# Performance work log

Measured on AMD Instinct MI355X. Metric: run time of the kernel, lower is better.

The kernel has to match this reference:

```python
import jax, jax.numpy as jnp
import numpy as np

B, S, E = 4, 1024, 1024
H, DH = 16, 64
P = 64  # prompt length
MASKED_BIAS = -10000.0


def setup_inputs() -> dict:
    key = jax.random.key(0)
    ks = jax.random.split(key, 9)
    return {
        "hidden_states": jax.random.normal(ks[0], (B, S, E), jnp.float32),
        "promptKey": jax.random.normal(ks[1], (B, H, P, DH), jnp.float32),
        "promptValue": jax.random.normal(ks[2], (B, H, P, DH), jnp.float32),
        "textualKey": jax.random.normal(ks[3], (B, H, S, DH), jnp.float32),
        "textualValue": jax.random.normal(ks[4], (B, H, S, DH), jnp.float32),
        "promptMask": jnp.ones((B, 1, S, P), jnp.bool_),
        "c_attn_w": jax.random.normal(ks[5], (E, 3 * E), jnp.float32) * 0.02,
        "c_attn_b": jnp.zeros((3 * E,), jnp.float32),
        "c_proj_w": jax.random.normal(ks[6], (E, E), jnp.float32) * 0.02,
        "c_proj_b": jnp.zeros((E,), jnp.float32),
    }


def _split_heads(t):
    # [B, S, E] -> [B, H, S, DH]
    b, s, _ = t.shape
    return t.reshape(b, s, H, DH).transpose(0, 2, 1, 3)


def reference(hidden_states, promptKey, promptValue, textualKey, textualValue,
              promptMask, c_attn_w, c_attn_b, c_proj_w, c_proj_b):
    qkv = hidden_states @ c_attn_w + c_attn_b          # [B,S,3E]
    q, k, v = jnp.split(qkv, 3, axis=-1)
    q, k, v = _split_heads(q), _split_heads(k), _split_heads(v)  # [B,H,S,DH]

    # scores against prompt KV, textual KV, and elementwise self term
    promptW = jnp.einsum("bhsd,bhpd->bhsp", q, promptKey)       # [B,H,S,P]
    textW = jnp.einsum("bhsd,bhtd->bhst", q, textualKey)        # [B,H,S,S]
    selfW = jnp.sum(q * k, axis=-1, keepdims=True)              # [B,H,S,1]
    attn_weights = jnp.concatenate((promptW, textW, selfW), axis=-1)
    attn_weights = attn_weights / jnp.sqrt(jnp.float32(DH))

    # non-residual causal mask: bias[qlen-qlen:qlen, 1:klen+1] -> strictly lower tri
    causal = jnp.tri(S, S, -1, dtype=bool)                      # [S,S]
    self_mask = jnp.ones((S, 1), dtype=bool)
    causal_self = jnp.concatenate((causal, self_mask), axis=-1)[None, None]  # [1,1,S,S+1]
    full_mask = jnp.concatenate(
        (promptMask, jnp.broadcast_to(causal_self, (B, 1, S, S + 1))), axis=-1)
    attn_weights = jnp.where(full_mask, attn_weights, MASKED_BIAS)
    attn_weights = jax.nn.softmax(attn_weights, axis=-1)

    wSelf = attn_weights[..., -1:]                              # [B,H,S,1]
    wRest = attn_weights[..., :-1]                              # [B,H,S,P+S]
    valuePast = jnp.concatenate((promptValue, textualValue), axis=-2)  # [B,H,P+S,DH]
    attn_output = jnp.einsum("bhsk,bhkd->bhsd", wRest, valuePast) + wSelf * v

    # merge heads and output projection
    attn_output = attn_output.transpose(0, 2, 1, 3).reshape(B, S, E)
    return attn_output @ c_proj_w + c_proj_b
```

## Files before the change

### kernel.cpp

```cpp
#include <hip/hip_runtime.h>
#include <hip/hip_bf16.h>
#include <stdint.h>

#define H_ 16
#define DH_ 64
#define S_ 1024
#define B_ 4
#define E_ 1024
#define P_ 64
#define BH_ (B_ * H_)
#define KV_ (P_ + S_)
#define NT_ 17
#define TILE_ELEMS 4096

typedef __attribute__((ext_vector_type(8))) short short8;
typedef __attribute__((ext_vector_type(4))) float floatx4;

#define MFMA_BF16(a, b, c) __builtin_amdgcn_mfma_f32_16x16x32_bf16((a), (b), (c), 0, 0, 0)

__device__ __forceinline__ float bf2f(unsigned short u) {
    union { float f; uint32_t i; } x;
    x.i = ((uint32_t)u) << 16;
    return x.f;
}
__device__ __forceinline__ unsigned short f2bf(float f) {
    uint32_t i = __float_as_uint(f);
    uint32_t r = (i + 0x7fffu + ((i >> 16) & 1u)) >> 16;
    return (unsigned short)r;
}

__device__ __forceinline__ void gl_lds16(const void* g, void* l) {
    __builtin_amdgcn_global_load_lds(
        (const __attribute__((address_space(1))) uint32_t*)g,
        (__attribute__((address_space(3))) uint32_t*)l, 16, 0, 0);
}

#define BARRIER() asm volatile("s_barrier" ::: "memory")
#define WAIT_VM(n) asm volatile("s_waitcnt vmcnt(" #n ")" ::: "memory")
#define LGKM0() asm volatile("s_waitcnt lgkmcnt(0)" ::: "memory")

__global__ void prep(const float* __restrict__ hidden, const float* __restrict__ cw,
                     const float* __restrict__ pw, const float* __restrict__ pK,
                     const float* __restrict__ tK, const float* __restrict__ pV,
                     const float* __restrict__ tV, unsigned short* __restrict__ Ah,
                     unsigned short* __restrict__ Wt1, unsigned short* __restrict__ Wt2,
                     unsigned short* __restrict__ Kp, unsigned short* __restrict__ Vp) {
    __shared__ float t[32][33];
    int bid = blockIdx.x, tid = threadIdx.x;
    if (bid < 4096) {
        int i = bid * 256 + tid;
        float4 v = ((const float4*)hidden)[i];
        ushort4 o;
        o.x = f2bf(v.x); o.y = f2bf(v.y); o.z = f2bf(v.z); o.w = f2bf(v.w);
        ((ushort4*)Ah)[i] = o;
    } else if (bid < 8192) {
        const float* in; unsigned short* out; int R, C, bxx, byy;
        if (bid < 7168) { int i = bid - 4096; in = cw; out = Wt1; R = 1024; C = 3072; bxx = i % 96; byy = i / 96; }
        else            { int i = bid - 7168; in = pw; out = Wt2; R = 1024; C = 1024; bxx = i % 32; byy = i / 32; }
        int tx = tid & 31, ty = tid >> 5;
        int c0 = bxx * 32, r0 = byy * 32;
#pragma unroll
        for (int i = 0; i < 4; ++i)
            t[ty + i * 8][tx] = in[(size_t)(r0 + ty + i * 8) * C + c0 + tx];
        __syncthreads();
#pragma unroll
        for (int i = 0; i < 4; ++i)
            out[(size_t)(c0 + ty + i * 8) * R + r0 + tx] = f2bf(t[tx][ty + i * 8]);
    } else {
        int gid0 = (bid - 8192) * 256 + tid;
        int half = gid0 / (BH_ * 8704);
        int gid = gid0 % (BH_ * 8704);
        int bh = gid / 8704, rem = gid % 8704;
        int tt = rem / 512, r2 = rem % 512;
        int f = r2 >> 6, lane = r2 & 63;
        int nt = f >> 1, h = f & 1, quad = lane >> 4, cl = lane & 15;
        unsigned short o[8];
        if (half == 0) {
            int key = tt * 64 + nt * 16 + cl;
            int dh = h * 32 + quad * 8;
            const float* src = (key < P_)
                ? pK + ((size_t)bh * P_ + key) * DH_ + dh
                : tK + ((size_t)bh * S_ + (key - P_)) * DH_ + dh;
#pragma unroll
            for (int u = 0; u < 8; ++u) o[u] = f2bf(src[u]);
            *(int4*)&Kp[(size_t)gid * 8] = *(int4*)o;
        } else {
            int dhn = nt * 16 + cl;
            int kbase = tt * 64 + h * 32 + quad * 8;
            const float* src = (kbase < P_)
                ? pV + ((size_t)bh * P_ + kbase) * DH_ + dhn
                : tV + ((size_t)bh * S_ + (kbase - P_)) * DH_ + dhn;
#pragma unroll
            for (int u = 0; u < 8; ++u) o[u] = f2bf(src[(size_t)u * DH_]);
            *(int4*)&Vp[(size_t)gid * 8] = *(int4*)o;
        }
    }
}

template <int MODE, int TM, int TN, int BK>
__global__ __launch_bounds__(256) void gemm_bt(
    const unsigned short* __restrict__ A, const unsigned short* __restrict__ Bt,
    const float* __restrict__ bias, float* __restrict__ Cout,
    unsigned short* __restrict__ Qo, unsigned short* __restrict__ Ko,
    unsigned short* __restrict__ Vo, int M, int N, int K) {
    constexpr int MI = TM / 32, NI = TN / 32;
    constexpr int NA = TM * BK / 2048;
    constexpr int NB = TN * BK / 2048;
    static_assert(NA + NB == 4, "vmcnt constant assumes 4 loads/tile");
    __shared__ __align__(16) unsigned short lA[2][TM * BK];
    __shared__ __align__(16) unsigned short lB[2][TN * BK];
    int tid = threadIdx.x;
    int wave = tid >> 6, lane = tid & 63, quad = lane >> 4, cl = lane & 15;
    int m0 = blockIdx.y * TM, n0 = blockIdx.x * TN;
    int wm = (wave >> 1) * (TM / 2), wn = (wave & 1) * (TN / 2);
    floatx4 acc[MI][NI];
#pragma unroll
    for (int mi = 0; mi < MI; ++mi)
#pragma unroll
        for (int ni = 0; ni < NI; ++ni) acc[mi][ni] = (floatx4){0.f, 0.f, 0.f, 0.f};

    auto issue = [&](int k0, int buf) {
#pragma unroll
        for (int li = 0; li < NA; ++li) {
            int o = (li * 256 + tid) * 16;
            int hh = o / (TM * 64), rr = (o % (TM * 64)) >> 6, c8 = (o >> 4) & 3;
            gl_lds16(A + (size_t)(m0 + rr) * K + k0 + hh * 32 + c8 * 8,
                     (char*)lA[buf] + o);
        }
#pragma unroll
        for (int li = 0; li < NB; ++li) {
            int o = (li * 256 + tid) * 16;
            int hh = o / (TN * 64), rr = (o % (TN * 64)) >> 6, c8 = (o >> 4) & 3;
            gl_lds16(Bt + (size_t)(n0 + rr) * K + k0 + hh * 32 + c8 * 8,
                     (char*)lB[buf] + o);
        }
    };
    auto compute = [&](int buf) {
#pragma unroll
        for (int kk = 0; kk < BK / 32; ++kk) {
            short8 af[MI], bfr[NI];
#pragma unroll
            for (int mi = 0; mi < MI; ++mi)
                af[mi] = *(const short8*)&lA[buf][kk * TM * 32 + (wm + mi * 16 + cl) * 32 + quad * 8];
#pragma unroll
            for (int ni = 0; ni < NI; ++ni)
                bfr[ni] = *(const short8*)&lB[buf][kk * TN * 32 + (wn + ni * 16 + cl) * 32 + quad * 8];
#pragma unroll
            for (int mi = 0; mi < MI; ++mi)
#pragma unroll
                for (int ni = 0; ni < NI; ++ni)
                    acc[mi][ni] = MFMA_BF16(af[mi], bfr[ni], acc[mi][ni]);
        }
    };

    int nT = K / BK;
    issue(0, 0);
    for (int t = 0; t < nT; ++t) {
        int buf = t & 1;
        if (t + 1 < nT) {
            issue((t + 1) * BK, buf ^ 1);
            WAIT_VM(4);
        } else {
            WAIT_VM(0);
        }
        BARRIER();
        compute(buf);
        BARRIER();
    }

#pragma unroll
    for (int ni = 0; ni < NI; ++ni) {
        int ncol = n0 + wn + ni * 16 + cl;
        float bv = bias[ncol];
#pragma unroll
        for (int mi = 0; mi < MI; ++mi) {
#pragma unroll
            for (int r = 0; r < 4; ++r) {
                int mrow = m0 + wm + mi * 16 + quad * 4 + r;
                float v = acc[mi][ni][r] + bv;
                if (MODE == 0) {
                    Cout[(size_t)mrow * N + ncol] = v;
                } else {
                    int which = ncol >> 10, e = ncol & 1023;
                    int hh = e >> 6, dh = e & 63;
                    int b = mrow >> 10, s = mrow & 1023;
                    size_t idx = ((size_t)(b * H_ + hh) * S_ + s) * DH_ + dh;
                    unsigned short* dst = (which == 0) ? Qo : ((which == 1) ? Ko : Vo);
                    dst[idx] = f2bf(v);
                }
            }
        }
    }
}

__global__ __launch_bounds__(512, 2) void gemm8_qkv(
    const unsigned short* __restrict__ A, const unsigned short* __restrict__ Bt,
    const float* __restrict__ bias, unsigned short* __restrict__ Qo,
    unsigned short* __restrict__ Ko, unsigned short* __restrict__ Vo,
    int M, int N, int K, int nbx) {
    __shared__ __align__(16) unsigned short sm[4][16384];
    int tid = threadIdx.x;
    int wave = tid >> 6, lane = tid & 63, quad = lane >> 4, cl = lane & 15;
    int cpx = gridDim.x >> 3;
    int swzb = ((int)blockIdx.x & 7) * cpx + ((int)blockIdx.x >> 3);
    int m0 = (swzb / nbx) * 256, n0 = (swzb % nbx) * 256;
    int wm = (wave >> 2) * 128, wn = (wave & 3) * 64;
    int cq = quad ^ ((cl >> 1) & 3);

    auto stage = [&](const unsigned short* __restrict__ G, int row0, int k0,
                     unsigned short* l) {
#pragma unroll
        for (int li = 0; li < 4; ++li) {
            int idx = li * 512 + tid;
            int kh = idx >> 10;
            int r = (idx >> 2) & 255;
            int c = (idx & 3) ^ ((r >> 1) & 3);
            gl_lds16(G + (size_t)(row0 + r) * K + k0 + kh * 32 + c * 8,
                     (char*)l + idx * 16);
        }
    };

    floatx4 acc[8][4];
#pragma unroll
    for (int mi = 0; mi < 8; ++mi)
#pragma unroll
        for (int ni = 0; ni < 4; ++ni) acc[mi][ni] = (floatx4){0.f, 0.f, 0.f, 0.f};

    int nT = K / 64;
    stage(A, m0, 0, sm[0]);
    stage(Bt, n0, 0, sm[1]);
    WAIT_VM(0);
    BARRIER();

    for (int j = 0; j < nT; ++j) {
        const unsigned short* sa = sm[(j & 1) * 2];
        const unsigned short* sb = sm[(j & 1) * 2 + 1];
        unsigned short* na = sm[((j & 1) ^ 1) * 2];
        unsigned short* nb = sm[((j & 1) ^ 1) * 2 + 1];
        short8 af[4], bf0[4], bf1[4];

#pragma unroll
        for (int ni = 0; ni < 4; ++ni)
            bf0[ni] = *(const short8*)(sb + (wn + ni * 16 + cl) * 32 + cq * 8);
#pragma unroll
        for (int mi = 0; mi < 4; ++mi)
            af[mi] = *(const short8*)(sa + (wm + mi * 16 + cl) * 32 + cq * 8);
        if (j + 1 < nT) stage(A, m0, (j + 1) * 64, na);
        BARRIER(); LGKM0();
        __builtin_amdgcn_s_setprio(1);
#pragma unroll
        for (int mi = 0; mi < 4; ++mi)
#pragma unroll
            for (int ni = 0; ni < 4; ++ni)
                acc[mi][ni] = MFMA_BF16(af[mi], bf0[ni], acc[mi][ni]);
        __builtin_amdgcn_s_setprio(0);
        BARRIER();

#pragma unroll
        for (int ni = 0; ni < 4; ++ni)
            bf1[ni] = *(const short8*)(sb + 8192 + (wn + ni * 16 + cl) * 32 + cq * 8);
#pragma unroll
        for (int mi = 0; mi < 4; ++mi)
            af[mi] = *(const short8*)(sa + 8192 + (wm + mi * 16 + cl) * 32 + cq * 8);
        if (j + 1 < nT) stage(Bt, n0, (j + 1) * 64, nb);
        BARRIER(); LGKM0();
        __builtin_amdgcn_s_setprio(1);
#pragma unroll
        for (int mi = 0; mi < 4; ++mi)
#pragma unroll
            for (int ni = 0; ni < 4; ++ni)
                acc[mi][ni] = MFMA_BF16(af[mi], bf1[ni], acc[mi][ni]);
        __builtin_amdgcn_s_setprio(0);
        BARRIER();

#pragma unroll
        for (int mi = 0; mi < 4; ++mi)
            af[mi] = *(const short8*)(sa + (wm + 64 + mi * 16 + cl) * 32 + cq * 8);
        BARRIER(); LGKM0();
        __builtin_amdgcn_s_setprio(1);
#pragma unroll
        for (int mi = 0; mi < 4; ++mi)
#pragma unroll
            for (int ni = 0; ni < 4; ++ni)
                acc[4 + mi][ni] = MFMA_BF16(af[mi], bf0[ni], acc[4 + mi][ni]);
        __builtin_amdgcn_s_setprio(0);
        BARRIER();

#pragma unroll
        for (int mi = 0; mi < 4; ++mi)
            af[mi] = *(const short8*)(sa + 8192 + (wm + 64 + mi * 16 + cl) * 32 + cq * 8);
        BARRIER(); LGKM0();
        __builtin_amdgcn_s_setprio(1);
#pragma unroll
        for (int mi = 0; mi < 4; ++mi)
#pragma unroll
            for (int ni = 0; ni < 4; ++ni)
                acc[4 + mi][ni] = MFMA_BF16(af[mi], bf1[ni], acc[4 + mi][ni]);
        __builtin_amdgcn_s_setprio(0);
        WAIT_VM(0);
        BARRIER();
    }

#pragma unroll
    for (int ni = 0; ni < 4; ++ni) {
        int ncol = n0 + wn + ni * 16 + cl;
        float bv = bias[ncol];
        int which = ncol >> 10, e = ncol & 1023;
        int hh = e >> 6, dh = e & 63;
        unsigned short* dst = (which == 0) ? Qo : ((which == 1) ? Ko : Vo);
#pragma unroll
        for (int mi = 0; mi < 8; ++mi) {
#pragma unroll
            for (int r = 0; r < 4; ++r) {
                int mrow = m0 + wm + mi * 16 + quad * 4 + r;
                int b = mrow >> 10, s = mrow & 1023;
                dst[((size_t)(b * H_ + hh) * S_ + s) * DH_ + dh] =
                    f2bf(acc[mi][ni][r] + bv);
            }
        }
    }
}

__global__ __launch_bounds__(256) void attn_k(
    const unsigned short* __restrict__ Q, const unsigned short* __restrict__ Kc,
    const unsigned short* __restrict__ Vc, const unsigned short* __restrict__ Kp,
    const unsigned short* __restrict__ Vp, unsigned short* __restrict__ Aout) {
    __shared__ __align__(16) unsigned short lK[2][TILE_ELEMS];
    __shared__ __align__(16) unsigned short lV[2][TILE_ELEMS];
    __shared__ __align__(16) unsigned short lP[4][16 * 72];
    int tid = threadIdx.x, wave = tid >> 6, lane = tid & 63;
    int quad = lane >> 4, cl = lane & 15;
    int l = blockIdx.x;
    int p = l >> 6, bh = l & 63;
    int b = bh >> 4, h = bh & 15;
    const unsigned short* Qb = Q + (size_t)bh * S_ * DH_;
    const unsigned short* Kb = Kc + (size_t)bh * S_ * DH_;
    const unsigned short* Vb = Vc + (size_t)bh * S_ * DH_;
    const unsigned short* Kpb = Kp + (size_t)bh * NT_ * TILE_ELEMS;
    const unsigned short* Vpb = Vp + (size_t)bh * NT_ * TILE_ELEMS;
    unsigned short* lp = lP[wave];
    int so = wave * 1024 + lane * 16;

    int x1 = p, x2 = 15 - p;
    int qb1 = x1 * 64 + wave * 16, qb2 = x2 * 64 + wave * 16;

    short8 a0_1 = *(const short8*)(Qb + (size_t)(qb1 + cl) * DH_ + quad * 8);
    short8 a1_1 = *(const short8*)(Qb + (size_t)(qb1 + cl) * DH_ + quad * 8 + 32);
    short8 a0_2 = *(const short8*)(Qb + (size_t)(qb2 + cl) * DH_ + quad * 8);
    short8 a1_2 = *(const short8*)(Qb + (size_t)(qb2 + cl) * DH_ + quad * 8 + 32);

    float lsum1[4] = {0.f, 0.f, 0.f, 0.f}, lsum2[4] = {0.f, 0.f, 0.f, 0.f};
    floatx4 O1[4], O2[4];
#pragma unroll
    for (int nt = 0; nt < 4; ++nt) {
        O1[nt] = (floatx4){0.f, 0.f, 0.f, 0.f};
        O2[nt] = (floatx4){0.f, 0.f, 0.f, 0.f};
    }

    int rl = wave * 16 + quad * 4;

    auto issue_tile = [&](int t, int bi) {
        const char* gK = (const char*)(Kpb + (size_t)t * TILE_ELEMS);
        const char* gV = (const char*)(Vpb + (size_t)t * TILE_ELEMS);
        gl_lds16(gK + so, (char*)lK[bi] + so);
        gl_lds16(gK + 4096 + so, (char*)lK[bi] + 4096 + so);
        gl_lds16(gV + so, (char*)lV[bi] + so);
        gl_lds16(gV + 4096 + so, (char*)lV[bi] + 4096 + so);
    };

    auto do_tile = [&](const unsigned short* Kt, const unsigned short* Vt,
                       short8 a0, short8 a1, floatx4* O, float* lsum, bool diag) {
        floatx4 s[4];
#pragma unroll
        for (int nt = 0; nt < 4; ++nt) {
            s[nt] = (floatx4){0.f, 0.f, 0.f, 0.f};
            short8 k0 = *(const short8*)&Kt[(nt * 2 + 0) * 512 + lane * 8];
            short8 k1 = *(const short8*)&Kt[(nt * 2 + 1) * 512 + lane * 8];
            s[nt] = MFMA_BF16(a0, k0, s[nt]);
            s[nt] = MFMA_BF16(a1, k1, s[nt]);
        }
#pragma unroll
        for (int nt = 0; nt < 4; ++nt) {
            int col = nt * 16 + cl;
#pragma unroll
            for (int r = 0; r < 4; ++r) {
                float v = s[nt][r] * 0.125f;
                if (diag && col >= rl + r) v = -10000.0f;
                float pb = __expf(v);
                lsum[r] += pb;
                lp[(quad * 4 + r) * 72 + col] = f2bf(pb);
            }
        }
        asm volatile("s_waitcnt lgkmcnt(0)" ::: "memory");
        short8 p0 = *(const short8*)&lp[cl * 72 + quad * 8];
        short8 p1 = *(const short8*)&lp[cl * 72 + quad * 8 + 32];
#pragma unroll
        for (int nt = 0; nt < 4; ++nt) {
            short8 v0 = *(const short8*)&Vt[(nt * 2 + 0) * 512 + lane * 8];
            short8 v1 = *(const short8*)&Vt[(nt * 2 + 1) * 512 + lane * 8];
            O[nt] = MFMA_BF16(p0, v0, O[nt]);
            O[nt] = MFMA_BF16(p1, v1, O[nt]);
        }
    };

    int T1 = x1 + 2, Tu = x2 + 2;
    issue_tile(0, 0);
    for (int t = 0; t < Tu; ++t) {
        int bi = t & 1;
        if (t + 1 < Tu) {
            issue_tile(t + 1, bi ^ 1);
            WAIT_VM(4);
        } else {
            WAIT_VM(0);
        }
        BARRIER();

        do_tile(lK[bi], lV[bi], a0_2, a1_2, O2, lsum2, t == Tu - 1);
        if (t < T1) do_tile(lK[bi], lV[bi], a0_1, a1_1, O1, lsum1, t == T1 - 1);
        BARRIER();
    }

#pragma unroll
    for (int seg = 0; seg < 2; ++seg) {
        int qb = seg ? qb2 : qb1;
        float* lsum = seg ? lsum2 : lsum1;
        floatx4* O = seg ? O2 : O1;
#pragma unroll
        for (int r = 0; r < 4; ++r) {
            float rs = lsum[r];
            rs += __shfl_xor(rs, 1, 16);
            rs += __shfl_xor(rs, 2, 16);
            rs += __shfl_xor(rs, 4, 16);
            rs += __shfl_xor(rs, 8, 16);
            int row = qb + quad * 4 + r;
            const unsigned short* qp = Qb + (size_t)row * DH_ + cl * 4;
            const unsigned short* kp = Kb + (size_t)row * DH_ + cl * 4;
            float d = 0.f;
#pragma unroll
            for (int u = 0; u < 4; ++u) d += bf2f(qp[u]) * bf2f(kp[u]);
            d += __shfl_xor(d, 1, 16);
            d += __shfl_xor(d, 2, 16);
            d += __shfl_xor(d, 4, 16);
            d += __shfl_xor(d, 8, 16);
            float ps = __expf(d * 0.125f);
            float linv = 1.0f / (rs + ps);
#pragma unroll
            for (int nt = 0; nt < 4; ++nt) {
                float vv = bf2f(Vb[(size_t)row * DH_ + nt * 16 + cl]);
                float o = (O[nt][r] + ps * vv) * linv;
                Aout[((size_t)b * S_ + row) * E_ + h * DH_ + nt * 16 + cl] = f2bf(o);
            }
        }
    }
}

extern "C" void kernel_launch(void* const* d_in, const int* in_sizes, int n_in,
                              void* d_out, int out_size, void* d_ws, size_t ws_size,
                              hipStream_t stream) {
    const float* hidden = (const float*)d_in[0];
    const float* pK = (const float*)d_in[1];
    const float* pV = (const float*)d_in[2];
    const float* tK = (const float*)d_in[3];
    const float* tV = (const float*)d_in[4];
    const float* cw = (const float*)d_in[6];
    const float* cb = (const float*)d_in[7];
    const float* pw = (const float*)d_in[8];
    const float* pb = (const float*)d_in[9];
    float* out = (float*)d_out;

    unsigned short* ws = (unsigned short*)d_ws;
    unsigned short* Wt1 = ws;
    unsigned short* Wt2 = Wt1 + (size_t)3072 * 1024;
    unsigned short* Ah  = Wt2 + (size_t)1024 * 1024;
    unsigned short* Qw  = Ah + (size_t)4096 * 1024;
    unsigned short* Kw  = Qw + (size_t)BH_ * S_ * DH_;
    unsigned short* Vw  = Kw + (size_t)BH_ * S_ * DH_;
    unsigned short* Kp  = Vw + (size_t)BH_ * S_ * DH_;
    unsigned short* Vp  = Kp + (size_t)BH_ * NT_ * TILE_ELEMS;
    unsigned short* At  = Ah;

    prep<<<12544, 256, 0, stream>>>(hidden, cw, pw, pK, tK, pV, tV,
                                    Ah, Wt1, Wt2, Kp, Vp);
    gemm8_qkv<<<192, 512, 0, stream>>>(Ah, Wt1, cb, Qw, Kw, Vw, 4096, 3072, 1024, 12);
    attn_k<<<512, 256, 0, stream>>>(Qw, Kw, Vw, Kp, Vp, At);
    gemm_bt<0, 128, 128, 32><<<dim3(1024 / 128, 4096 / 128), 256, 0, stream>>>(
        At, Wt2, pb, out, nullptr, nullptr, nullptr, 4096, 1024, 1024);
}
```

Before: 209.7 us.

## Deepen QKV GEMM pipeline to 4-stage K=32 ring and retile output projection

The QKV GEMM moves from a double-buffered K=64 tile to a four-slot ring of K=32 tiles prefetched three steps ahead, with graded vmcnt waits so each step waits only for its own tile. The goal is more overlap of global-to-LDS loads with MFMA work and fewer barriers per K step. This comes with more loop iterations and per-iteration sync overhead. Separately, the output projection GEMM is launched with 64x64 tiles and a larger grid instead of 128x128, trading per-block reuse for more blocks in flight.

```diff
diff --git a/kernel.cpp b/kernel.cpp
--- a/kernel.cpp
+++ b/kernel.cpp
@@ -198,7 +198,8 @@
     const float* __restrict__ bias, unsigned short* __restrict__ Qo,
     unsigned short* __restrict__ Ko, unsigned short* __restrict__ Vo,
     int M, int N, int K, int nbx) {
-    __shared__ __align__(16) unsigned short sm[4][16384];
+    __shared__ __align__(16) unsigned short smA[4][8192];
+    __shared__ __align__(16) unsigned short smB[4][8192];
     int tid = threadIdx.x;
     int wave = tid >> 6, lane = tid & 63, quad = lane >> 4, cl = lane & 15;
     int cpx = gridDim.x >> 3;
@@ -210,12 +211,11 @@
     auto stage = [&](const unsigned short* __restrict__ G, int row0, int k0,
                      unsigned short* l) {
 #pragma unroll
-        for (int li = 0; li < 4; ++li) {
+        for (int li = 0; li < 2; ++li) {
             int idx = li * 512 + tid;
-            int kh = idx >> 10;
-            int r = (idx >> 2) & 255;
+            int r = idx >> 2;
             int c = (idx & 3) ^ ((r >> 1) & 3);
-            gl_lds16(G + (size_t)(row0 + r) * K + k0 + kh * 32 + c * 8,
+            gl_lds16(G + (size_t)(row0 + r) * K + k0 + c * 8,
                      (char*)l + idx * 16);
         }
     };
@@ -226,78 +226,50 @@
 #pragma unroll
         for (int ni = 0; ni < 4; ++ni) acc[mi][ni] = (floatx4){0.f, 0.f, 0.f, 0.f};
 
-    int nT = K / 64;
-    stage(A, m0, 0, sm[0]);
-    stage(Bt, n0, 0, sm[1]);
-    WAIT_VM(0);
+    int nT = K / 32;
+    stage(A, m0, 0, smA[0]);  stage(Bt, n0, 0, smB[0]);
+    stage(A, m0, 32, smA[1]); stage(Bt, n0, 32, smB[1]);
+    stage(A, m0, 64, smA[2]); stage(Bt, n0, 64, smB[2]);
+    WAIT_VM(8);
     BARRIER();
 
     for (int j = 0; j < nT; ++j) {
-        const unsigned short* sa = sm[(j & 1) * 2];
-        const unsigned short* sb = sm[(j & 1) * 2 + 1];
-        unsigned short* na = sm[((j & 1) ^ 1) * 2];
-        unsigned short* nb = sm[((j & 1) ^ 1) * 2 + 1];
-        short8 af[4], bf0[4], bf1[4];
+        const unsigned short* sa = smA[j & 3];
+        const unsigned short* sb = smB[j & 3];
+        short8 af[4], bfr[4];
 
 #pragma unroll
         for (int ni = 0; ni < 4; ++ni)
-            bf0[ni] = *(const short8*)(sb + (wn + ni * 16 + cl) * 32 + cq * 8);
+            bfr[ni] = *(const short8*)(sb + (wn + ni * 16 + cl) * 32 + cq * 8);
 #pragma unroll
         for (int mi = 0; mi < 4; ++mi)
             af[mi] = *(const short8*)(sa + (wm + mi * 16 + cl) * 32 + cq * 8);
-        if (j + 1 < nT) stage(A, m0, (j + 1) * 64, na);
+        if (j + 3 < nT) stage(A, m0, (j + 3) * 32, smA[(j + 3) & 3]);
         BARRIER(); LGKM0();
         __builtin_amdgcn_s_setprio(1);
 #pragma unroll
         for (int mi = 0; mi < 4; ++mi)
 #pragma unroll
             for (int ni = 0; ni < 4; ++ni)
-                acc[mi][ni] = MFMA_BF16(af[mi], bf0[ni], acc[mi][ni]);
+                acc[mi][ni] = MFMA_BF16(af[mi], bfr[ni], acc[mi][ni]);
         __builtin_amdgcn_s_setprio(0);
         BARRIER();
 
 #pragma unroll
-        for (int ni = 0; ni < 4; ++ni)
-            bf1[ni] = *(const short8*)(sb + 8192 + (wn + ni * 16 + cl) * 32 + cq * 8);
-#pragma unroll
         for (int mi = 0; mi < 4; ++mi)
-            af[mi] = *(const short8*)(sa + 8192 + (wm + mi * 16 + cl) * 32 + cq * 8);
-        if (j + 1 < nT) stage(Bt, n0, (j + 1) * 64, nb);
+            af[mi] = *(const short8*)(sa + (wm + 64 + mi * 16 + cl) * 32 + cq * 8);
+        if (j + 3 < nT) stage(Bt, n0, (j + 3) * 32, smB[(j + 3) & 3]);
         BARRIER(); LGKM0();
         __builtin_amdgcn_s_setprio(1);
 #pragma unroll
         for (int mi = 0; mi < 4; ++mi)
 #pragma unroll
             for (int ni = 0; ni < 4; ++ni)
-                acc[mi][ni] = MFMA_BF16(af[mi], bf1[ni], acc[mi][ni]);
+                acc[4 + mi][ni] = MFMA_BF16(af[mi], bfr[ni], acc[4 + mi][ni]);
         __builtin_amdgcn_s_setprio(0);
-        BARRIER();
-
-#pragma unroll
-        for (int mi = 0; mi < 4; ++mi)
-            af[mi] = *(const short8*)(sa + (wm + 64 + mi * 16 + cl) * 32 + cq * 8);
-        BARRIER(); LGKM0();
-        __builtin_amdgcn_s_setprio(1);
-#pragma unroll
-        for (int mi = 0; mi < 4; ++mi)
-#pragma unroll
-            for (int ni = 0; ni < 4; ++ni)
-                acc[4 + mi][ni] = MFMA_BF16(af[mi], bf0[ni], acc[4 + mi][ni]);
-        __builtin_amdgcn_s_setprio(0);
-        BARRIER();
-
-#pragma unroll
-        for (int mi = 0; mi < 4; ++mi)
-            af[mi] = *(const short8*)(sa + 8192 + (wm + 64 + mi * 16 + cl) * 32 + cq * 8);
-        BARRIER(); LGKM0();
-        __builtin_amdgcn_s_setprio(1);
-#pragma unroll
-        for (int mi = 0; mi < 4; ++mi)
-#pragma unroll
-            for (int ni = 0; ni < 4; ++ni)
-                acc[4 + mi][ni] = MFMA_BF16(af[mi], bf1[ni], acc[4 + mi][ni]);
-        __builtin_amdgcn_s_setprio(0);
-        WAIT_VM(0);
+        if (j + 3 < nT)      { WAIT_VM(8); }
+        else if (j + 2 < nT) { WAIT_VM(4); }
+        else if (j + 1 < nT) { WAIT_VM(0); }
         BARRIER();
     }
 
@@ -483,6 +455,6 @@
                                     Ah, Wt1, Wt2, Kp, Vp);
     gemm8_qkv<<<192, 512, 0, stream>>>(Ah, Wt1, cb, Qw, Kw, Vw, 4096, 3072, 1024, 12);
     attn_k<<<512, 256, 0, stream>>>(Qw, Kw, Vw, Kp, Vp, At);
-    gemm_bt<0, 128, 128, 32><<<dim3(1024 / 128, 4096 / 128), 256, 0, stream>>>(
+    gemm_bt<0, 64, 64, 64><<<dim3(1024 / 64, 4096 / 128 * 2), 256, 0, stream>>>(
         At, Wt2, pb, out, nullptr, nullptr, nullptr, 4096, 1024, 1024);
 }
```

After: 207.8 us. About the same (-0.9%).
